# Kernel optimization log

Hardware: AMD Instinct MI355X
Metric: run time of the kernel (lower is better)

Reference implementation:

```python
import jax, jax.numpy as jnp
import numpy as np

B, V, T, C, HIN, WIN = 1, 6, 3, 256, 32, 32
NH = 8
LN_EPS = 1e-5


def setup_inputs() -> dict:
    key = jax.random.key(0)
    ks = jax.random.split(key, 14)
    s = 0.02
    lim = 1.0 / np.sqrt(C)
    def lin_w(k):
        return jax.random.uniform(k, (C, C), jnp.float32, -lim, lim)
    return {
        "history_feats": jax.random.normal(ks[0], (B, V, T, C, HIN, WIN), jnp.float32),
        "query_embed": jax.random.normal(ks[1], (1, C, 1, 1), jnp.float32) * s,
        "camera_pos_embed": jax.random.normal(ks[2], (V, C), jnp.float32) * s,
        "temporal_pos_embed": jax.random.normal(ks[3], (T, C), jnp.float32) * s,
        "spatial_pos_embed": jax.random.normal(ks[4], (1, C, 1, 1), jnp.float32) * s,
        "q_w": lin_w(ks[5]), "q_b": jnp.zeros((C,), jnp.float32),
        "k_w": lin_w(ks[6]), "k_b": jnp.zeros((C,), jnp.float32),
        "v_w": lin_w(ks[7]), "v_b": jnp.zeros((C,), jnp.float32),
        "o_w": lin_w(ks[8]), "o_b": jnp.zeros((C,), jnp.float32),
        "ln_g": jnp.ones((C,), jnp.float32),
        "ln_b": jnp.zeros((C,), jnp.float32),
        "query_cam_idx": 0,
        "H": 32,
        "W": 32,
    }


def reference(history_feats, query_embed, camera_pos_embed, temporal_pos_embed,
              spatial_pos_embed, q_w, q_b, k_w, k_b, v_w, v_b, o_w, o_b,
              ln_g, ln_b, query_cam_idx, H, W):
    B_, V_, T_, C_, Hin, Win = history_feats.shape
    dh = C_ // NH
    # --- build query: [B, H*W, C] ---
    q = query_embed + camera_pos_embed[query_cam_idx][None, :, None, None] + spatial_pos_embed
    q = jnp.broadcast_to(q, (B_, C_, H, W)).reshape(B_, C_, H * W).transpose(0, 2, 1)
    kv = (history_feats
          + temporal_pos_embed[None, None, :, :, None, None]
          + camera_pos_embed[None, :, None, :, None, None])
    kv = kv.transpose(0, 1, 2, 4, 5, 3).reshape(B_, V_ * T_ * Hin * Win, C_)
    # --- projections (torch Linear: x @ W.T + b) ---
    qp = q @ q_w.T + q_b
    kp = kv @ k_w.T + k_b
    vp = kv @ v_w.T + v_b
    # --- split heads: [B, NH, L, dh] ---
    qh = qp.reshape(B_, H * W, NH, dh).transpose(0, 2, 1, 3)
    kh = kp.reshape(B_, -1, NH, dh).transpose(0, 2, 1, 3)
    vh = vp.reshape(B_, -1, NH, dh).transpose(0, 2, 1, 3)
    scale = float(dh) ** -0.5
    attn = jax.nn.softmax(jnp.einsum('bhqd,bhkd->bhqk', qh, kh) * scale, axis=-1)
    out = jnp.einsum('bhqk,bhkd->bhqd', attn, vh)
    out = out.transpose(0, 2, 1, 3).reshape(B_, H * W, C_)
    out = out @ o_w.T + o_b
    # --- LayerNorm over channel dim ---
    mu = out.mean(-1, keepdims=True)
    var = ((out - mu) ** 2).mean(-1, keepdims=True)
    out = (out - mu) * jax.lax.rsqrt(var + LN_EPS) * ln_g + ln_b
    return out.transpose(0, 2, 1).reshape(B_, C_, H, W)
```

## Files before the change

kernel.cpp:

```cpp
#include <hip/hip_runtime.h>
#include <hip/hip_fp16.h>

typedef const float* fcp;

#define C_    256
#define NH_   8
#define DH_   32
#define VT_   18
#define HWK   1024
#define L_    (VT_*HWK)
#define SCALE_ 0.17677669529663687f

#define EMB_OFF  0
#define WF_OFF   4608
#define BB_OFF   6656
#define PS_OFF   6720
#define Y_OFF    9024
#define Z_OFF    9280
#define CTXP_OFF 9536

__device__ __forceinline__ float blockReduceSum256(float v){
  __shared__ float red[4];
  #pragma unroll
  for (int off = 32; off; off >>= 1) v += __shfl_xor(v, off, 64);
  const int lane = threadIdx.x & 63, w = threadIdx.x >> 6;
  __syncthreads();
  if (lane == 0) red[w] = v;
  __syncthreads();
  return red[0] + red[1] + red[2] + red[3];
}

__global__ void k_fold(fcp qe, fcp cam, fcp tpe, fcp spe, const int* __restrict__ cidx,
                       fcp qw, fcp qb, fcp kw, fcp kb, float* __restrict__ ws){
  __shared__ float qvS[C_];
  __shared__ float qpS[DH_];
  const int b = blockIdx.x, t = threadIdx.x, lane = t & 63, wv = t >> 6;
  const int ci = cidx[0];
  qvS[t] = qe[t] + cam[ci*C_ + t] + spe[t];
  {
    const int v = b/3, tt = b - v*3;
    ws[EMB_OFF + b*C_ + t] = tpe[tt*C_ + t] + cam[v*C_ + t];
  }
  __syncthreads();
  if (b < 8){
    #pragma unroll
    for (int i = 0; i < 8; i++){
      const int r = b*DH_ + wv*8 + i;
      fcp qr = qw + (size_t)r*C_;
      float v = qr[lane]*qvS[lane] + qr[64+lane]*qvS[64+lane]
              + qr[128+lane]*qvS[128+lane] + qr[192+lane]*qvS[192+lane];
      #pragma unroll
      for (int off = 32; off; off >>= 1) v += __shfl_xor(v, off, 64);
      if (lane == 0) qpS[wv*8 + i] = v + qb[r];
    }
    __syncthreads();
    float acc = 0.f;
    #pragma unroll 8
    for (int d = 0; d < DH_; d++)
      acc += qpS[d] * kw[(size_t)(b*DH_ + d)*C_ + t];
    ws[WF_OFF + b*C_ + t] = SCALE_ * acc;
    if (t == 0){
      float bb = 0.f;
      for (int d = 0; d < DH_; d++) bb += qpS[d] * kb[b*DH_ + d];
      ws[BB_OFF + b] = SCALE_ * bb;
    }
  }
}

__global__ void k_attn(fcp feats, float* __restrict__ ws){
  __shared__ __align__(16) float wf[C_*8];
  __shared__ float redS[32];
  __shared__ float basef[8];
  __shared__ __align__(16) float pred[8*512];
  __shared__ float pexS[64*8];
  __shared__ __half fS[8*32*66];
  const int bid = blockIdx.x, vt = bid >> 4, sc = bid & 15, t = threadIdx.x;

  for (int idx = t; idx < 2048; idx += 512){
    const int h = idx >> 8, c = idx & 255;
    wf[c*8 + h] = ws[WF_OFF + idx];
  }
  __syncthreads();
  if (t < 256){
    const float e = ws[EMB_OFF + vt*C_ + t];
    const float4 wa = *(const float4*)&wf[t*8];
    const float4 wb = *(const float4*)&wf[t*8 + 4];
    float pb[8] = {e*wa.x, e*wa.y, e*wa.z, e*wa.w, e*wb.x, e*wb.y, e*wb.z, e*wb.w};
    #pragma unroll
    for (int h = 0; h < 8; h++){
      float v = pb[h];
      #pragma unroll
      for (int off = 32; off; off >>= 1) v += __shfl_xor(v, off, 64);
      if ((t & 63) == 0) redS[(t >> 6)*8 + h] = v;
    }
  }
  __syncthreads();
  if (t < 8) basef[t] = redS[t] + redS[8+t] + redS[16+t] + redS[24+t] + ws[BB_OFF + t];
  __syncthreads();
  const int s = t & 63, cg = t >> 6;
  fcp fp = feats + ((size_t)vt*C_ + cg*32)*HWK + sc*64 + s;
  float acc[8] = {0,0,0,0,0,0,0,0};
  #pragma unroll 8
  for (int i = 0; i < 32; i++){
    const float fv = fp[(size_t)i*HWK];
    fS[(cg*32 + i)*66 + s] = __float2half(fv);
    const float4 wa = *(const float4*)&wf[(cg*32+i)*8];
    const float4 wb = *(const float4*)&wf[(cg*32+i)*8 + 4];
    acc[0] += fv*wa.x; acc[1] += fv*wa.y; acc[2] += fv*wa.z; acc[3] += fv*wa.w;
    acc[4] += fv*wb.x; acc[5] += fv*wb.y; acc[6] += fv*wb.z; acc[7] += fv*wb.w;
  }
  #pragma unroll
  for (int h = 0; h < 8; h++) pred[cg*512 + h*64 + s] = acc[h];
  __syncthreads();
  {
    const int h1 = t >> 6, tok = t & 63;
    float sum = basef[h1];
    #pragma unroll
    for (int cg2 = 0; cg2 < 8; cg2++) sum += pred[cg2*512 + t];
    const float e = __expf(sum);
    pexS[tok*8 + h1] = e;
    float v = e;
    #pragma unroll
    for (int off = 32; off; off >>= 1) v += __shfl_xor(v, off, 64);
    if (tok == 0) ws[PS_OFF + bid*8 + h1] = v;
  }
  __syncthreads();
  const int lane = t & 63, hB = lane & 7, isub = lane >> 3;
  float aB[4] = {0.f, 0.f, 0.f, 0.f};
  #pragma unroll 8
  for (int s2 = 0; s2 < 64; s2++){
    const float pe = pexS[s2*8 + hB];
    #pragma unroll
    for (int p = 0; p < 4; p++)
      aB[p] += pe * __half2float(fS[(cg*32 + p*8 + isub)*66 + s2]);
  }
  float* outp = ws + CTXP_OFF + (size_t)bid*2048;
  #pragma unroll
  for (int p = 0; p < 4; p++)
    outp[hB*256 + cg*32 + p*8 + isub] = aB[p];
}

__global__ void k_vproj(fcp vw, fcp vb, float* __restrict__ ws){
  __shared__ float psS[288*8];
  const int r = blockIdx.x, t = threadIdx.x, h = r >> 5;
  for (int i = t; i < 288*8; i += 256) psS[i] = ws[PS_OFF + i];
  __syncthreads();
  float ctx = 0.f;
  const float* pp = ws + CTXP_OFF + h*256 + t;
  #pragma unroll 8
  for (int b = 0; b < 288; b++) ctx += pp[(size_t)b*2048];
  float denom = 0.f, embP = 0.f;
  for (int vt = 0; vt < VT_; vt++){
    float P = 0.f;
    #pragma unroll
    for (int sc2 = 0; sc2 < 16; sc2++) P += psS[(vt*16 + sc2)*8 + h];
    denom += P;
    embP  += ws[EMB_OFF + vt*C_ + t] * P;
  }
  const float ctxn = (ctx + embP) / denom;
  float v = vw[(size_t)r*C_ + t] * ctxn;
  v = blockReduceSum256(v);
  if (t == 0) ws[Y_OFF + r] = v + vb[r];
}

__global__ void k_oproj(fcp ow, fcp ob, float* __restrict__ ws){
  const int r = blockIdx.x, t = threadIdx.x;
  float v = ow[(size_t)r*C_ + t] * ws[Y_OFF + t];
  v = blockReduceSum256(v);
  if (t == 0) ws[Z_OFF + r] = v + ob[r];
}

__global__ void k_out(fcp lng, fcp lnb, const float* __restrict__ ws,
                      float* __restrict__ out, int hw){
  const int c = blockIdx.x, t = threadIdx.x;
  const float z = ws[Z_OFF + t];
  const float s  = blockReduceSum256(z);
  const float s2 = blockReduceSum256(z*z);
  const float mu = s * (1.f/C_);
  const float var = s2 * (1.f/C_) - mu*mu;
  const float rs = rsqrtf(var + 1e-5f);
  const float fin = (ws[Z_OFF + c] - mu) * rs * lng[c] + lnb[c];
  float4 pk = make_float4(fin, fin, fin, fin);
  ((float4*)(out + (size_t)c*hw))[t] = pk;
}

extern "C" void kernel_launch(void* const* d_in, const int* in_sizes, int n_in,
                              void* d_out, int out_size, void* d_ws, size_t ws_size,
                              hipStream_t stream) {
  fcp feats = (fcp)d_in[0];
  fcp qe    = (fcp)d_in[1];
  fcp cam   = (fcp)d_in[2];
  fcp tpe   = (fcp)d_in[3];
  fcp spe   = (fcp)d_in[4];
  fcp qw    = (fcp)d_in[5];
  fcp qb    = (fcp)d_in[6];
  fcp kw    = (fcp)d_in[7];
  fcp kb    = (fcp)d_in[8];
  fcp vw    = (fcp)d_in[9];
  fcp vb    = (fcp)d_in[10];
  fcp ow    = (fcp)d_in[11];
  fcp ob    = (fcp)d_in[12];
  fcp lng   = (fcp)d_in[13];
  fcp lnb   = (fcp)d_in[14];
  const int* cidx = (const int*)d_in[15];
  float* ws = (float*)d_ws;
  float* out = (float*)d_out;
  const int hw = out_size / C_;

  k_fold  <<<18,  256, 0, stream>>>(qe, cam, tpe, spe, cidx, qw, qb, kw, kb, ws);
  k_attn  <<<288, 512, 0, stream>>>(feats, ws);
  k_vproj <<<256, 256, 0, stream>>>(vw, vb, ws);
  k_oproj <<<256, 256, 0, stream>>>(ow, ob, ws);
  k_out   <<<256, 256, 0, stream>>>(lng, lnb, ws, out, hw);
}
```

Before: 148.2 us.

## Fold V and O projections into one matrix and atomically reduce context

Precomputes the per-head product of the output and value weights (plus the combined bias) in the first kernel, so the separate V-projection and O-projection kernels become a single z-projection kernel. The attention kernel now accumulates its per-block context partials straight into one buffer with atomicAdd, removing the 288-way strided reduction pass. LayerNorm sums are also gathered atomically so the final kernel skips its block reductions. In exchange, the fold kernel grows to 256 blocks, each doing a 256x256 weight product, and float atomics make the summation order nondeterministic.

```diff
diff --git a/kernel.cpp b/kernel.cpp
--- a/kernel.cpp
+++ b/kernel.cpp
@@ -8,16 +8,18 @@
 #define DH_   32
 #define VT_   18
 #define HWK   1024
-#define L_    (VT_*HWK)
 #define SCALE_ 0.17677669529663687f
 
-#define EMB_OFF  0
-#define WF_OFF   4608
-#define BB_OFF   6656
-#define PS_OFF   6720
-#define Y_OFF    9024
-#define Z_OFF    9280
-#define CTXP_OFF 9536
+#define QP_OFF   0
+#define EMB_OFF  256
+#define WF_OFF   4864
+#define BB_OFF   6912
+#define PS_OFF   6920
+#define CTX_OFF  9224
+#define B2_OFF   11272
+#define Z_OFF    11528
+#define SUM_OFF  11784
+#define W2_OFF   12288
 
 __device__ __forceinline__ float blockReduceSum256(float v){
   __shared__ float red[4];
@@ -31,16 +33,21 @@
 }
 
 __global__ void k_fold(fcp qe, fcp cam, fcp tpe, fcp spe, const int* __restrict__ cidx,
-                       fcp qw, fcp qb, fcp kw, fcp kb, float* __restrict__ ws){
+                       fcp qw, fcp qb, fcp kw, fcp kb, fcp vw, fcp vb, fcp ow, fcp ob,
+                       float* __restrict__ ws){
   __shared__ float qvS[C_];
   __shared__ float qpS[DH_];
+  __shared__ float owS[C_];
   const int b = blockIdx.x, t = threadIdx.x, lane = t & 63, wv = t >> 6;
   const int ci = cidx[0];
   qvS[t] = qe[t] + cam[ci*C_ + t] + spe[t];
-  {
+  owS[t] = ow[(size_t)b*C_ + t];
+  if (b < VT_){
     const int v = b/3, tt = b - v*3;
     ws[EMB_OFF + b*C_ + t] = tpe[tt*C_ + t] + cam[v*C_ + t];
   }
+  if (b >= 18 && b < 26) ws[CTX_OFF + (b-18)*C_ + t] = 0.f;
+  if (b == 26 && t < 2) ws[SUM_OFF + t] = 0.f;
   __syncthreads();
   if (b < 8){
     #pragma unroll
@@ -64,6 +71,22 @@
       for (int d = 0; d < DH_; d++) bb += qpS[d] * kb[b*DH_ + d];
       ws[BB_OFF + b] = SCALE_ * bb;
     }
+  }
+  {
+    float acc[8] = {0,0,0,0,0,0,0,0};
+    #pragma unroll 8
+    for (int hd = 0; hd < 256; hd++){
+      const float wsc = owS[hd];
+      acc[hd >> 5] += wsc * vw[(size_t)hd*C_ + t];
+    }
+    float* wrow = ws + W2_OFF + (size_t)b*2048;
+    #pragma unroll
+    for (int h = 0; h < 8; h++) wrow[h*256 + t] = acc[h];
+  }
+  {
+    float v2 = owS[t] * vb[t];
+    v2 = blockReduceSum256(v2);
+    if (t == 0) ws[B2_OFF + b] = v2 + ob[b];
   }
 }
 
@@ -75,6 +98,7 @@
   __shared__ float pexS[64*8];
   __shared__ __half fS[8*32*66];
   const int bid = blockIdx.x, vt = bid >> 4, sc = bid & 15, t = threadIdx.x;
+  const int s = t & 63, cgi = t >> 6;
 
   for (int idx = t; idx < 2048; idx += 512){
     const int h = idx >> 8, c = idx & 255;
@@ -97,20 +121,21 @@
   __syncthreads();
   if (t < 8) basef[t] = redS[t] + redS[8+t] + redS[16+t] + redS[24+t] + ws[BB_OFF + t];
   __syncthreads();
-  const int s = t & 63, cg = t >> 6;
-  fcp fp = feats + ((size_t)vt*C_ + cg*32)*HWK + sc*64 + s;
-  float acc[8] = {0,0,0,0,0,0,0,0};
-  #pragma unroll 8
-  for (int i = 0; i < 32; i++){
-    const float fv = fp[(size_t)i*HWK];
-    fS[(cg*32 + i)*66 + s] = __float2half(fv);
-    const float4 wa = *(const float4*)&wf[(cg*32+i)*8];
-    const float4 wb = *(const float4*)&wf[(cg*32+i)*8 + 4];
-    acc[0] += fv*wa.x; acc[1] += fv*wa.y; acc[2] += fv*wa.z; acc[3] += fv*wa.w;
-    acc[4] += fv*wb.x; acc[5] += fv*wb.y; acc[6] += fv*wb.z; acc[7] += fv*wb.w;
-  }
-  #pragma unroll
-  for (int h = 0; h < 8; h++) pred[cg*512 + h*64 + s] = acc[h];
+  {
+    fcp fp = feats + ((size_t)vt*C_ + cgi*32)*HWK + sc*64 + s;
+    float acc[8] = {0,0,0,0,0,0,0,0};
+    #pragma unroll 8
+    for (int i = 0; i < 32; i++){
+      const float fv = fp[(size_t)i*HWK];
+      fS[(cgi*32 + i)*66 + s] = __float2half(fv);
+      const float4 wa = *(const float4*)&wf[(cgi*32+i)*8];
+      const float4 wb = *(const float4*)&wf[(cgi*32+i)*8 + 4];
+      acc[0] += fv*wa.x; acc[1] += fv*wa.y; acc[2] += fv*wa.z; acc[3] += fv*wa.w;
+      acc[4] += fv*wb.x; acc[5] += fv*wb.y; acc[6] += fv*wb.z; acc[7] += fv*wb.w;
+    }
+    #pragma unroll
+    for (int h = 0; h < 8; h++) pred[cgi*512 + h*64 + s] = acc[h];
+  }
   __syncthreads();
   {
     const int h1 = t >> 6, tok = t & 63;
@@ -125,59 +150,76 @@
     if (tok == 0) ws[PS_OFF + bid*8 + h1] = v;
   }
   __syncthreads();
-  const int lane = t & 63, hB = lane & 7, isub = lane >> 3;
-  float aB[4] = {0.f, 0.f, 0.f, 0.f};
-  #pragma unroll 8
-  for (int s2 = 0; s2 < 64; s2++){
-    const float pe = pexS[s2*8 + hB];
+  {
+    const int lane = t & 63, hB = lane & 7, isub = lane >> 3;
+    float aB[4] = {0.f, 0.f, 0.f, 0.f};
+    #pragma unroll 8
+    for (int s2 = 0; s2 < 64; s2++){
+      const float pe = pexS[s2*8 + hB];
+      #pragma unroll
+      for (int p = 0; p < 4; p++)
+        aB[p] += pe * __half2float(fS[(cgi*32 + p*8 + isub)*66 + s2]);
+    }
     #pragma unroll
     for (int p = 0; p < 4; p++)
-      aB[p] += pe * __half2float(fS[(cg*32 + p*8 + isub)*66 + s2]);
-  }
-  float* outp = ws + CTXP_OFF + (size_t)bid*2048;
+      atomicAdd(ws + CTX_OFF + hB*256 + cgi*32 + p*8 + isub, aB[p]);
+  }
+}
+
+__global__ void k_zproj(float* __restrict__ ws){
+  __shared__ float psS[288*8];
+  __shared__ float Ps[VT_*8];
+  __shared__ float denomS[8];
+  __shared__ __align__(16) float ctxnS[2048];
+  const int o = blockIdx.x, t = threadIdx.x;
+  for (int i = t; i < 288*8; i += 256) psS[i] = ws[PS_OFF + i];
+  __syncthreads();
+  if (t < VT_*8){
+    const int vt = t >> 3, h = t & 7;
+    float p = 0.f;
+    #pragma unroll
+    for (int s2 = 0; s2 < 16; s2++) p += psS[(vt*16 + s2)*8 + h];
+    Ps[t] = p;
+  }
+  __syncthreads();
+  if (t < 8){
+    float d = 0.f;
+    #pragma unroll
+    for (int vt = 0; vt < VT_; vt++) d += Ps[vt*8 + t];
+    denomS[t] = d;
+  }
+  __syncthreads();
+  {
+    float embP[8] = {0,0,0,0,0,0,0,0};
+    #pragma unroll 2
+    for (int vt = 0; vt < VT_; vt++){
+      const float e = ws[EMB_OFF + vt*C_ + t];
+      #pragma unroll
+      for (int h = 0; h < 8; h++) embP[h] += e * Ps[vt*8 + h];
+    }
+    #pragma unroll
+    for (int h = 0; h < 8; h++)
+      ctxnS[h*256 + t] = (ws[CTX_OFF + h*256 + t] + embP[h]) / denomS[h];
+  }
+  __syncthreads();
+  float v = 0.f;
+  const float* wrow = ws + W2_OFF + (size_t)o*2048;
   #pragma unroll
-  for (int p = 0; p < 4; p++)
-    outp[hB*256 + cg*32 + p*8 + isub] = aB[p];
-}
-
-__global__ void k_vproj(fcp vw, fcp vb, float* __restrict__ ws){
-  __shared__ float psS[288*8];
-  const int r = blockIdx.x, t = threadIdx.x, h = r >> 5;
-  for (int i = t; i < 288*8; i += 256) psS[i] = ws[PS_OFF + i];
-  __syncthreads();
-  float ctx = 0.f;
-  const float* pp = ws + CTXP_OFF + h*256 + t;
-  #pragma unroll 8
-  for (int b = 0; b < 288; b++) ctx += pp[(size_t)b*2048];
-  float denom = 0.f, embP = 0.f;
-  for (int vt = 0; vt < VT_; vt++){
-    float P = 0.f;
-    #pragma unroll
-    for (int sc2 = 0; sc2 < 16; sc2++) P += psS[(vt*16 + sc2)*8 + h];
-    denom += P;
-    embP  += ws[EMB_OFF + vt*C_ + t] * P;
-  }
-  const float ctxn = (ctx + embP) / denom;
-  float v = vw[(size_t)r*C_ + t] * ctxn;
+  for (int k = 0; k < 8; k++) v += wrow[k*256 + t] * ctxnS[k*256 + t];
   v = blockReduceSum256(v);
-  if (t == 0) ws[Y_OFF + r] = v + vb[r];
-}
-
-__global__ void k_oproj(fcp ow, fcp ob, float* __restrict__ ws){
-  const int r = blockIdx.x, t = threadIdx.x;
-  float v = ow[(size_t)r*C_ + t] * ws[Y_OFF + t];
-  v = blockReduceSum256(v);
-  if (t == 0) ws[Z_OFF + r] = v + ob[r];
+  if (t == 0){
+    const float z = v + ws[B2_OFF + o];
+    ws[Z_OFF + o] = z;
+    atomicAdd(ws + SUM_OFF, z);
+    atomicAdd(ws + SUM_OFF + 1, z*z);
+  }
 }
 
 __global__ void k_out(fcp lng, fcp lnb, const float* __restrict__ ws,
                       float* __restrict__ out, int hw){
   const int c = blockIdx.x, t = threadIdx.x;
-  const float z = ws[Z_OFF + t];
-  const float s  = blockReduceSum256(z);
-  const float s2 = blockReduceSum256(z*z);
-  const float mu = s * (1.f/C_);
-  const float var = s2 * (1.f/C_) - mu*mu;
+  const float mu  = ws[SUM_OFF] * (1.f/C_);
+  const float var = ws[SUM_OFF + 1] * (1.f/C_) - mu*mu;
   const float rs = rsqrtf(var + 1e-5f);
   const float fin = (ws[Z_OFF + c] - mu) * rs * lng[c] + lnb[c];
   float4 pk = make_float4(fin, fin, fin, fin);
@@ -207,9 +249,9 @@
   float* out = (float*)d_out;
   const int hw = out_size / C_;
 
-  k_fold  <<<18,  256, 0, stream>>>(qe, cam, tpe, spe, cidx, qw, qb, kw, kb, ws);
-  k_attn  <<<288, 512, 0, stream>>>(feats, ws);
-  k_vproj <<<256, 256, 0, stream>>>(vw, vb, ws);
-  k_oproj <<<256, 256, 0, stream>>>(ow, ob, ws);
-  k_out   <<<256, 256, 0, stream>>>(lng, lnb, ws, out, hw);
-}
+  k_fold <<<256, 256, 0, stream>>>(qe, cam, tpe, spe, cidx, qw, qb, kw, kb,
+                                   vw, vb, ow, ob, ws);
+  k_attn <<<288, 512, 0, stream>>>(feats, ws);
+  k_zproj<<<256, 256, 0, stream>>>(ws);
+  k_out  <<<256, 256, 0, stream>>>(lng, lnb, ws, out, hw);
+}
```

Result: slower. 152.4 us (+2.8%).

## Fuse query/key fold into attention kernel and merge o-proj with LayerNorm output

Applied to the files above, without the earlier changes.

Removes the separate fold kernel by having every attention block recompute the query projection and folded key weights, and merges the output projection with the LayerNorm/broadcast kernel, dropping five launches to three. Each attention block now does a redundant 256x256 matvec plus a 32x8x256 fold (per-thread row reads of qw, poorly coalesced). Every tail block likewise recomputes the full output projection. The intent is to cut launch and inter-kernel gaps at the price of extra redundant compute and weight traffic per block.

```diff
diff --git a/kernel.cpp b/kernel.cpp
--- a/kernel.cpp
+++ b/kernel.cpp
@@ -8,16 +8,11 @@
 #define DH_   32
 #define VT_   18
 #define HWK   1024
-#define L_    (VT_*HWK)
 #define SCALE_ 0.17677669529663687f
 
-#define EMB_OFF  0
-#define WF_OFF   4608
-#define BB_OFF   6656
-#define PS_OFF   6720
-#define Y_OFF    9024
-#define Z_OFF    9280
-#define CTXP_OFF 9536
+#define PS_OFF   0
+#define Y_OFF    2304
+#define CTXP_OFF 4096
 
 __device__ __forceinline__ float blockReduceSum256(float v){
   __shared__ float red[4];
@@ -30,59 +25,57 @@
   return red[0] + red[1] + red[2] + red[3];
 }
 
-__global__ void k_fold(fcp qe, fcp cam, fcp tpe, fcp spe, const int* __restrict__ cidx,
-                       fcp qw, fcp qb, fcp kw, fcp kb, float* __restrict__ ws){
+__global__ void __launch_bounds__(512, 4)
+k_attn(fcp feats, fcp qe, fcp cam, fcp tpe, fcp spe, const int* __restrict__ cidx,
+       fcp qw, fcp qb, fcp kw, fcp kb, float* __restrict__ ws){
   __shared__ float qvS[C_];
-  __shared__ float qpS[DH_];
-  const int b = blockIdx.x, t = threadIdx.x, lane = t & 63, wv = t >> 6;
-  const int ci = cidx[0];
-  qvS[t] = qe[t] + cam[ci*C_ + t] + spe[t];
-  {
-    const int v = b/3, tt = b - v*3;
-    ws[EMB_OFF + b*C_ + t] = tpe[tt*C_ + t] + cam[v*C_ + t];
-  }
-  __syncthreads();
-  if (b < 8){
-    #pragma unroll
-    for (int i = 0; i < 8; i++){
-      const int r = b*DH_ + wv*8 + i;
-      fcp qr = qw + (size_t)r*C_;
-      float v = qr[lane]*qvS[lane] + qr[64+lane]*qvS[64+lane]
-              + qr[128+lane]*qvS[128+lane] + qr[192+lane]*qvS[192+lane];
-      #pragma unroll
-      for (int off = 32; off; off >>= 1) v += __shfl_xor(v, off, 64);
-      if (lane == 0) qpS[wv*8 + i] = v + qb[r];
-    }
-    __syncthreads();
-    float acc = 0.f;
-    #pragma unroll 8
-    for (int d = 0; d < DH_; d++)
-      acc += qpS[d] * kw[(size_t)(b*DH_ + d)*C_ + t];
-    ws[WF_OFF + b*C_ + t] = SCALE_ * acc;
-    if (t == 0){
-      float bb = 0.f;
-      for (int d = 0; d < DH_; d++) bb += qpS[d] * kb[b*DH_ + d];
-      ws[BB_OFF + b] = SCALE_ * bb;
-    }
-  }
-}
-
-__global__ void k_attn(fcp feats, float* __restrict__ ws){
+  __shared__ float qpS[C_];
+  __shared__ float embS[C_];
   __shared__ __align__(16) float wf[C_*8];
+  __shared__ float bbS[8];
   __shared__ float redS[32];
   __shared__ float basef[8];
   __shared__ __align__(16) float pred[8*512];
   __shared__ float pexS[64*8];
   __shared__ __half fS[8*32*66];
   const int bid = blockIdx.x, vt = bid >> 4, sc = bid & 15, t = threadIdx.x;
-
-  for (int idx = t; idx < 2048; idx += 512){
-    const int h = idx >> 8, c = idx & 255;
-    wf[c*8 + h] = ws[WF_OFF + idx];
-  }
-  __syncthreads();
-  if (t < 256){
-    const float e = ws[EMB_OFF + vt*C_ + t];
+  const int s = t & 63, cgi = t >> 6;
+
+  if (t < 256){
+    const int ci = cidx[0];
+    qvS[t] = qe[t] + cam[ci*C_ + t] + spe[t];
+    const int v = vt/3, tt = vt - v*3;
+    embS[t] = tpe[tt*C_ + t] + cam[v*C_ + t];
+  }
+  __syncthreads();
+  if (t < 256){
+    fcp qr = qw + (size_t)t*C_;
+    float a = 0.f;
+    #pragma unroll 8
+    for (int k = 0; k < C_; k++) a += qr[k] * qvS[k];
+    qpS[t] = a + qb[t];
+  }
+  __syncthreads();
+  if (t < 256){
+    float facc[8] = {0,0,0,0,0,0,0,0};
+    #pragma unroll 4
+    for (int d = 0; d < DH_; d++){
+      #pragma unroll
+      for (int h = 0; h < 8; h++)
+        facc[h] += qpS[h*DH_ + d] * kw[(size_t)(h*DH_ + d)*C_ + t];
+    }
+    #pragma unroll
+    for (int h = 0; h < 8; h++) wf[t*8 + h] = SCALE_ * facc[h];
+  }
+  if (t >= 256 && t < 264){
+    const int h = t - 256;
+    float bb = 0.f;
+    for (int d = 0; d < DH_; d++) bb += qpS[h*DH_ + d] * kb[h*DH_ + d];
+    bbS[h] = SCALE_ * bb;
+  }
+  __syncthreads();
+  if (t < 256){
+    const float e = embS[t];
     const float4 wa = *(const float4*)&wf[t*8];
     const float4 wb = *(const float4*)&wf[t*8 + 4];
     float pb[8] = {e*wa.x, e*wa.y, e*wa.z, e*wa.w, e*wb.x, e*wb.y, e*wb.z, e*wb.w};
@@ -95,22 +88,23 @@
     }
   }
   __syncthreads();
-  if (t < 8) basef[t] = redS[t] + redS[8+t] + redS[16+t] + redS[24+t] + ws[BB_OFF + t];
-  __syncthreads();
-  const int s = t & 63, cg = t >> 6;
-  fcp fp = feats + ((size_t)vt*C_ + cg*32)*HWK + sc*64 + s;
-  float acc[8] = {0,0,0,0,0,0,0,0};
-  #pragma unroll 8
-  for (int i = 0; i < 32; i++){
-    const float fv = fp[(size_t)i*HWK];
-    fS[(cg*32 + i)*66 + s] = __float2half(fv);
-    const float4 wa = *(const float4*)&wf[(cg*32+i)*8];
-    const float4 wb = *(const float4*)&wf[(cg*32+i)*8 + 4];
-    acc[0] += fv*wa.x; acc[1] += fv*wa.y; acc[2] += fv*wa.z; acc[3] += fv*wa.w;
-    acc[4] += fv*wb.x; acc[5] += fv*wb.y; acc[6] += fv*wb.z; acc[7] += fv*wb.w;
-  }
-  #pragma unroll
-  for (int h = 0; h < 8; h++) pred[cg*512 + h*64 + s] = acc[h];
+  if (t < 8) basef[t] = redS[t] + redS[8+t] + redS[16+t] + redS[24+t] + bbS[t];
+  __syncthreads();
+  {
+    fcp fp = feats + ((size_t)vt*C_ + cgi*32)*HWK + sc*64 + s;
+    float acc[8] = {0,0,0,0,0,0,0,0};
+    #pragma unroll 8
+    for (int i = 0; i < 32; i++){
+      const float fv = fp[(size_t)i*HWK];
+      fS[(cgi*32 + i)*66 + s] = __float2half(fv);
+      const float4 wa = *(const float4*)&wf[(cgi*32+i)*8];
+      const float4 wb = *(const float4*)&wf[(cgi*32+i)*8 + 4];
+      acc[0] += fv*wa.x; acc[1] += fv*wa.y; acc[2] += fv*wa.z; acc[3] += fv*wa.w;
+      acc[4] += fv*wb.x; acc[5] += fv*wb.y; acc[6] += fv*wb.z; acc[7] += fv*wb.w;
+    }
+    #pragma unroll
+    for (int h = 0; h < 8; h++) pred[cgi*512 + h*64 + s] = acc[h];
+  }
   __syncthreads();
   {
     const int h1 = t >> 6, tok = t & 63;
@@ -125,61 +119,79 @@
     if (tok == 0) ws[PS_OFF + bid*8 + h1] = v;
   }
   __syncthreads();
-  const int lane = t & 63, hB = lane & 7, isub = lane >> 3;
-  float aB[4] = {0.f, 0.f, 0.f, 0.f};
-  #pragma unroll 8
-  for (int s2 = 0; s2 < 64; s2++){
-    const float pe = pexS[s2*8 + hB];
+  {
+    const int lane = t & 63, hB = lane & 7, isub = lane >> 3;
+    float aB[4] = {0.f, 0.f, 0.f, 0.f};
+    #pragma unroll 8
+    for (int s2 = 0; s2 < 64; s2++){
+      const float pe = pexS[s2*8 + hB];
+      #pragma unroll
+      for (int p = 0; p < 4; p++)
+        aB[p] += pe * __half2float(fS[(cgi*32 + p*8 + isub)*66 + s2]);
+    }
+    float* outp = ws + CTXP_OFF + (size_t)bid*2048;
     #pragma unroll
     for (int p = 0; p < 4; p++)
-      aB[p] += pe * __half2float(fS[(cg*32 + p*8 + isub)*66 + s2]);
-  }
-  float* outp = ws + CTXP_OFF + (size_t)bid*2048;
-  #pragma unroll
-  for (int p = 0; p < 4; p++)
-    outp[hB*256 + cg*32 + p*8 + isub] = aB[p];
-}
-
-__global__ void k_vproj(fcp vw, fcp vb, float* __restrict__ ws){
+      outp[hB*256 + cgi*32 + p*8 + isub] = aB[p];
+  }
+}
+
+__global__ void k_vproj(fcp tpe, fcp cam, fcp vw, fcp vb, float* __restrict__ ws){
   __shared__ float psS[288*8];
+  __shared__ float PvtR[VT_];
+  __shared__ float dR;
   const int r = blockIdx.x, t = threadIdx.x, h = r >> 5;
   for (int i = t; i < 288*8; i += 256) psS[i] = ws[PS_OFF + i];
+  __syncthreads();
+  if (t < VT_){
+    float p = 0.f;
+    #pragma unroll
+    for (int j = 0; j < 16; j++) p += psS[(t*16 + j)*8 + h];
+    PvtR[t] = p;
+  }
+  __syncthreads();
+  if (t == 0){
+    float d = 0.f;
+    #pragma unroll
+    for (int vt2 = 0; vt2 < VT_; vt2++) d += PvtR[vt2];
+    dR = d;
+  }
   __syncthreads();
   float ctx = 0.f;
   const float* pp = ws + CTXP_OFF + h*256 + t;
   #pragma unroll 8
-  for (int b = 0; b < 288; b++) ctx += pp[(size_t)b*2048];
-  float denom = 0.f, embP = 0.f;
-  for (int vt = 0; vt < VT_; vt++){
-    float P = 0.f;
-    #pragma unroll
-    for (int sc2 = 0; sc2 < 16; sc2++) P += psS[(vt*16 + sc2)*8 + h];
-    denom += P;
-    embP  += ws[EMB_OFF + vt*C_ + t] * P;
-  }
-  const float ctxn = (ctx + embP) / denom;
+  for (int b2 = 0; b2 < 288; b2++) ctx += pp[(size_t)b2*2048];
+  float embP = 0.f;
+  #pragma unroll 2
+  for (int vt2 = 0; vt2 < VT_; vt2++){
+    const int v2 = vt2/3, tt2 = vt2 - v2*3;
+    embP += (tpe[tt2*C_ + t] + cam[v2*C_ + t]) * PvtR[vt2];
+  }
+  const float ctxn = (ctx + embP) / dR;
   float v = vw[(size_t)r*C_ + t] * ctxn;
   v = blockReduceSum256(v);
   if (t == 0) ws[Y_OFF + r] = v + vb[r];
 }
 
-__global__ void k_oproj(fcp ow, fcp ob, float* __restrict__ ws){
-  const int r = blockIdx.x, t = threadIdx.x;
-  float v = ow[(size_t)r*C_ + t] * ws[Y_OFF + t];
-  v = blockReduceSum256(v);
-  if (t == 0) ws[Z_OFF + r] = v + ob[r];
-}
-
-__global__ void k_out(fcp lng, fcp lnb, const float* __restrict__ ws,
-                      float* __restrict__ out, int hw){
+__global__ void k_tailout(fcp ow, fcp ob, fcp lng, fcp lnb,
+                          const float* __restrict__ ws, float* __restrict__ out, int hw){
+  __shared__ float yS[C_];
+  __shared__ float zS[C_];
   const int c = blockIdx.x, t = threadIdx.x;
-  const float z = ws[Z_OFF + t];
-  const float s  = blockReduceSum256(z);
+  yS[t] = ws[Y_OFF + t];
+  __syncthreads();
+  fcp orow = ow + (size_t)t*C_;
+  float z = 0.f;
+  #pragma unroll 8
+  for (int k = 0; k < C_; k++) z += orow[k] * yS[k];
+  z += ob[t];
+  zS[t] = z;
+  const float s1 = blockReduceSum256(z);
   const float s2 = blockReduceSum256(z*z);
-  const float mu = s * (1.f/C_);
+  const float mu = s1 * (1.f/C_);
   const float var = s2 * (1.f/C_) - mu*mu;
   const float rs = rsqrtf(var + 1e-5f);
-  const float fin = (ws[Z_OFF + c] - mu) * rs * lng[c] + lnb[c];
+  const float fin = (zS[c] - mu) * rs * lng[c] + lnb[c];
   float4 pk = make_float4(fin, fin, fin, fin);
   ((float4*)(out + (size_t)c*hw))[t] = pk;
 }
@@ -207,9 +219,7 @@
   float* out = (float*)d_out;
   const int hw = out_size / C_;
 
-  k_fold  <<<18,  256, 0, stream>>>(qe, cam, tpe, spe, cidx, qw, qb, kw, kb, ws);
-  k_attn  <<<288, 512, 0, stream>>>(feats, ws);
-  k_vproj <<<256, 256, 0, stream>>>(vw, vb, ws);
-  k_oproj <<<256, 256, 0, stream>>>(ow, ob, ws);
-  k_out   <<<256, 256, 0, stream>>>(lng, lnb, ws, out, hw);
-}
+  k_attn   <<<288, 512, 0, stream>>>(feats, qe, cam, tpe, spe, cidx, qw, qb, kw, kb, ws);
+  k_vproj  <<<256, 256, 0, stream>>>(tpe, cam, vw, vb, ws);
+  k_tailout<<<256, 256, 0, stream>>>(ow, ob, lng, lnb, ws, out, hw);
+}
```

New measurement: 165.7 us. 1.12x slower.
